# Performance work log

Hardware: AMD Instinct MI355X
Metric: run time of the kernel (lower is better)

Reference implementation:

```python
import jax, jax.numpy as jnp
import numpy as np

N_NODES = 50000
N_EDGES = 800000
D = 256            # node_feat_size
D_EDGE = 16        # edge_feat_size (unused in forward math, as in the original)
G_FEAT = 200       # graph_feat_size
N_TASKS = 1
N_GRAPHS = 512


def _p(key, shape):
    return jax.random.normal(key, shape, dtype=jnp.float32) * 0.05


def setup_inputs() -> dict:
    key = jax.random.key(0)
    ks = jax.random.split(key, 24)
    inp = {
        'node_feats_1': jax.random.normal(ks[0], (N_NODES, D), dtype=jnp.float32),
        'edge_feats_1': jax.random.normal(ks[1], (N_EDGES, D_EDGE), dtype=jnp.float32),
        'node_feats_2': jax.random.normal(ks[2], (N_NODES, D), dtype=jnp.float32),
        'edge_feats_2': jax.random.normal(ks[3], (N_EDGES, D_EDGE), dtype=jnp.float32),
        'src_1': jax.random.randint(ks[4], (N_EDGES,), 0, N_NODES, dtype=jnp.int32),
        'dst_1': jax.random.randint(ks[5], (N_EDGES,), 0, N_NODES, dtype=jnp.int32),
        'graph_ids_1': jnp.sort(jax.random.randint(ks[6], (N_NODES,), 0, N_GRAPHS, dtype=jnp.int32)),
        'src_2': jax.random.randint(ks[7], (N_EDGES,), 0, N_NODES, dtype=jnp.int32),
        'dst_2': jax.random.randint(ks[8], (N_EDGES,), 0, N_NODES, dtype=jnp.int32),
        'graph_ids_2': jnp.sort(jax.random.randint(ks[9], (N_NODES,), 0, N_GRAPHS, dtype=jnp.int32)),
        # GCN layer 1 params (GraphConv weight/bias + residual Linear)
        'W1': _p(ks[10], (D, D)), 'b1': jnp.zeros((D,), jnp.float32),
        'Wr1': _p(ks[11], (D, D)), 'br1': jnp.zeros((D,), jnp.float32),
        # GCN layer 2 params
        'W2': _p(ks[12], (D, D)), 'b2': jnp.zeros((D,), jnp.float32),
        'Wr2': _p(ks[13], (D, D)), 'br2': jnp.zeros((D,), jnp.float32),
        # Readout 1 MLP
        'Ri1': _p(ks[14], (D, D)), 'rbi1': jnp.zeros((D,), jnp.float32),
        'Ro1': _p(ks[15], (D, G_FEAT)), 'rbo1': jnp.zeros((G_FEAT,), jnp.float32),
        # Readout 2 MLP
        'Ri2': _p(ks[16], (D, D)), 'rbi2': jnp.zeros((D,), jnp.float32),
        'Ro2': _p(ks[17], (D, G_FEAT)), 'rbo2': jnp.zeros((G_FEAT,), jnp.float32),
        # Predictor
        'Wp': _p(ks[18], (G_FEAT, N_TASKS)), 'bp': jnp.zeros((N_TASKS,), jnp.float32),
    }
    return inp


def _gcn_layer(h, src, dst, W, b, Wr, br):
    # DGL GraphConv, norm='none': project, aggregate (sum src->dst), bias, relu
    hW = h @ W                                             # [N, D]
    agg = jax.ops.segment_sum(jnp.take(hW, src, axis=0), dst, num_segments=N_NODES)
    conv = jax.nn.relu(agg + b)
    # residual branch: activation(Linear(h))
    res = jax.nn.relu(h @ Wr + br)
    return conv + res                                      # dropout=0, no batchnorm


def _readout(h, graph_ids, Wi, bi, Wo, bo):
    # MLPNodeReadout: Linear -> relu -> Linear, then sum over nodes per graph
    h = jax.nn.relu(h @ Wi + bi)
    h = h @ Wo + bo                                        # [N, G_FEAT]
    return jax.ops.segment_sum(h, graph_ids, num_segments=N_GRAPHS)


def reference(node_feats_1, edge_feats_1, node_feats_2, edge_feats_2,
              src_1, dst_1, graph_ids_1, src_2, dst_2, graph_ids_2,
              W1, b1, Wr1, br1, W2, b2, Wr2, br2,
              Ri1, rbi1, Ro1, rbo1, Ri2, rbi2, Ro2, rbo2, Wp, bp):
    h1 = _gcn_layer(node_feats_1, src_1, dst_1, W1, b1, Wr1, br1)
    g1 = _readout(h1, graph_ids_1, Ri1, rbi1, Ro1, rbo1)
    h2 = _gcn_layer(node_feats_2, src_2, dst_2, W2, b2, Wr2, br2)
    g2 = _readout(h2, graph_ids_2, Ri2, rbi2, Ro2, rbo2)
    g = g1 + g2                                            # [G, G_FEAT]
    return (g @ Wp + bp).reshape(-1)                       # [G * n_tasks]
```

## Files before the change

### kernel.cpp

```cpp
#include <hip/hip_runtime.h>

#define NN 50000
#define NE 800000
#define DD 256
#define GFEAT 200
#define NG 512

typedef __bf16 bf16;
typedef bf16 bf16x4 __attribute__((ext_vector_type(4)));
typedef bf16 bf16x8 __attribute__((ext_vector_type(8)));
typedef float f32x4 __attribute__((ext_vector_type(4)));

__device__ __forceinline__ void gl_lds16(const bf16* g, bf16* l) {
    __builtin_amdgcn_global_load_lds(
        (const __attribute__((address_space(1))) uint32_t*)(g),
        (__attribute__((address_space(3))) uint32_t*)(l), 16, 0, 0);
}

__device__ __forceinline__ bf16x8 frag_ld64(const bf16* s, int R, int C) {
    return *(const bf16x8*)&s[R * 64 + ((C ^ ((R >> 1) & 7)) << 3)];
}

#define EPI_STRIDE 136

__global__ __launch_bounds__(256) void conv_w8_kernel(
    const float* __restrict__ w0, const float* __restrict__ w1,
    const float* __restrict__ w2, const float* __restrict__ w3,
    const float* __restrict__ w4, const float* __restrict__ w5,
    const float* __restrict__ w6, const float* __restrict__ w7,
    bf16* __restrict__ out_base) {
    const float* ws[8] = {w0, w1, w2, w3, w4, w5, w6, w7};
    const int Ns[8] = {DD, DD, DD, GFEAT, DD, DD, DD, GFEAT};
    int m = blockIdx.y;
    const float* in = ws[m];
    int N = Ns[m];
    int idx = blockIdx.x * 256 + threadIdx.x;
    int n = idx >> 8, k = idx & 255;
    float v = (n < N) ? in[k * N + n] : 0.f;
    out_base[(size_t)m * 65536 + idx] = (bf16)v;
}

__global__ __launch_bounds__(256) void zero_g_kernel(float* __restrict__ G0,
                                                     float* __restrict__ G1) {
    float* G = blockIdx.y ? G1 : G0;
    int i = blockIdx.x * 256 + threadIdx.x;
    if (i < NG * GFEAT) G[i] = 0.f;
}

#define NBKT   128
#define NPB    391
#define NCHUNK 256
#define CE     ((NE + NCHUNK - 1) / NCHUNK)

__global__ __launch_bounds__(256) void csr_coarse_hist_kernel(
    const int* __restrict__ d0, const int* __restrict__ d1,
    int* __restrict__ cnt0, int* __restrict__ cnt1) {
    const int blk = blockIdx.x, t = threadIdx.x;
    const int* dst = blockIdx.y ? d1 : d0;
    int* cnt = blockIdx.y ? cnt1 : cnt0;
    __shared__ int hist[NBKT];
    if (t < NBKT) hist[t] = 0;
    __syncthreads();
    const int e0 = blk * CE;
    const int e1 = (e0 + CE < NE) ? e0 + CE : NE;
    for (int e = e0 + t; e < e1; e += 256)
        atomicAdd(&hist[dst[e] / NPB], 1);
    __syncthreads();
    if (t < NBKT) cnt[t * NCHUNK + blk] = hist[t];
}

__global__ __launch_bounds__(1024) void csr_scan_kernel(
    int* __restrict__ cnt0, int* __restrict__ cnt1,
    int* __restrict__ offs0, int* __restrict__ offs1) {
    int* cnt = blockIdx.y ? cnt1 : cnt0;
    const int t = threadIdx.x;
    const int PER = (NBKT * NCHUNK) / 1024;
    int v[PER];
    int sum = 0;
    const int base = t * PER;
#pragma unroll
    for (int i = 0; i < PER; i += 4) {
        int4 q = *(const int4*)&cnt[base + i];
        v[i] = q.x; v[i + 1] = q.y; v[i + 2] = q.z; v[i + 3] = q.w;
        sum += q.x + q.y + q.z + q.w;
    }
    __shared__ int s[1024];
    s[t] = sum;
    __syncthreads();
    for (int off = 1; off < 1024; off <<= 1) {
        int a = (t >= off) ? s[t - off] : 0;
        __syncthreads();
        s[t] += a;
        __syncthreads();
    }
    int run = s[t] - sum;
#pragma unroll
    for (int i = 0; i < PER; i++) { int c = v[i]; cnt[base + i] = run; run += c; }
    if (t == 0) (blockIdx.y ? offs1 : offs0)[NN] = NE;
}

__global__ __launch_bounds__(256) void csr_partition_kernel(
    const int* __restrict__ sA, const int* __restrict__ sB,
    const int* __restrict__ d0, const int* __restrict__ d1,
    const int* __restrict__ cnt0, const int* __restrict__ cnt1,
    int2* __restrict__ eb0, int2* __restrict__ eb1) {
    const int blk = blockIdx.x, t = threadIdx.x;
    const int* src = blockIdx.y ? sB : sA;
    const int* dst = blockIdx.y ? d1 : d0;
    const int* cnt = blockIdx.y ? cnt1 : cnt0;
    int2* eb = blockIdx.y ? eb1 : eb0;
    __shared__ int cur[NBKT];
    if (t < NBKT) cur[t] = cnt[t * NCHUNK + blk];
    __syncthreads();
    const int e0 = blk * CE;
    const int e1 = (e0 + CE < NE) ? e0 + CE : NE;
    for (int e = e0 + t; e < e1; e += 256) {
        int d = dst[e], s = src[e];
        int pos = atomicAdd(&cur[d / NPB], 1);
        eb[pos] = make_int2(s, d);
    }
}

__global__ __launch_bounds__(512) void csr_bucket_sort_kernel(
    const int* __restrict__ cnt0, const int* __restrict__ cnt1,
    const int2* __restrict__ eb0, const int2* __restrict__ eb1,
    int* __restrict__ offs0, int* __restrict__ offs1,
    int* __restrict__ csr0, int* __restrict__ csr1) {
    const int b = blockIdx.x, t = threadIdx.x;
    const int* cnt = blockIdx.y ? cnt1 : cnt0;
    const int2* eb = blockIdx.y ? eb1 : eb0;
    int* offs = blockIdx.y ? offs1 : offs0;
    int* csr = blockIdx.y ? csr1 : csr0;
    const int lo = b * NPB;
    const int ncnt = (NN - lo < NPB) ? (NN - lo) : NPB;
    const int beg = cnt[b * NCHUNK];
    const int end = (b == NBKT - 1) ? NE : cnt[(b + 1) * NCHUNK];

    __shared__ int hist[NPB];
    __shared__ int s[512];
    if (t < NPB) hist[t] = 0;
    __syncthreads();
    for (int i = beg + t; i < end; i += 512)
        atomicAdd(&hist[eb[i].y - lo], 1);
    __syncthreads();

    int h = (t < NPB) ? hist[t] : 0;
    s[t] = h;
    __syncthreads();
    for (int off = 1; off < 512; off <<= 1) {
        int a = (t >= off) ? s[t - off] : 0;
        __syncthreads();
        s[t] += a;
        __syncthreads();
    }
    int excl = s[t] - h;
    __syncthreads();
    if (t < NPB) hist[t] = excl;
    if (t < ncnt) offs[lo + t] = beg + excl;
    __syncthreads();

    for (int i = beg + t; i < end; i += 512) {
        int2 v = eb[i];
        int pos = atomicAdd(&hist[v.y - lo], 1);
        csr[beg + pos] = v.x;
    }
}


__global__ __launch_bounds__(512) void mfma_gemm2_kernel(
    const bf16* __restrict__ A0, const bf16* __restrict__ A1,
    const bf16* __restrict__ Bt0, const bf16* __restrict__ Bt1,
    const float* __restrict__ bias0, const float* __restrict__ bias1,
    bf16* __restrict__ out0, bf16* __restrict__ out1,
    int M, int Nb, int do_relu) {
    const int lid = blockIdx.x;
    const int r8 = lid & 7, cc = (lid >> 3) & 1, g = lid >> 4;
    const int row_blk = g * 8 + r8;
    if (row_blk * 256 >= M) return;
    const bf16* A = blockIdx.y ? A1 : A0;
    const bf16* Bt = blockIdx.y ? Bt1 : Bt0;
    const float* bias = blockIdx.y ? bias1 : bias0;
    bf16* out = blockIdx.y ? out1 : out0;

    __shared__ bf16 smem[24576];
    bf16* As = smem;
    bf16* Bs = smem + 16384;

    const int t    = threadIdx.x;
    const int lane = t & 63;
    const int w    = t >> 6;
    const int row0 = row_blk * 256;
    const int col0 = cc * 128;

    f32x4 acc[4][4] = {};
    const int wm = (w >> 1) * 64, wn = (w & 1) * 64;
    const int fm = lane & 15, fC = lane >> 4;

    for (int k0 = 0; k0 < 256; k0 += 64) {
#pragma unroll
        for (int r = 0; r < 4; r++) {
            int flat = r * 512 + t;
            int fr = flat >> 3, fc = flat & 7;
            int fcg = fc ^ ((fr >> 1) & 7);
            int arow = row0 + fr;
            if (arow > M - 1) arow = M - 1;
            gl_lds16(&A[(size_t)arow * 256 + k0 + fcg * 8], &As[flat * 8]);
        }
#pragma unroll
        for (int r = 0; r < 2; r++) {
            int flat = r * 512 + t;
            int fr = flat >> 3, fc = flat & 7;
            int fcg = fc ^ ((fr >> 1) & 7);
            int brow = col0 + fr;
            gl_lds16(&Bt[(size_t)brow * 256 + k0 + fcg * 8], &Bs[flat * 8]);
        }
        __syncthreads();
#pragma unroll
        for (int s = 0; s < 2; s++) {
            bf16x8 af[4], bfr[4];
#pragma unroll
            for (int i = 0; i < 4; i++) af[i] = frag_ld64(As, wm + i * 16 + fm, s * 4 + fC);
#pragma unroll
            for (int i = 0; i < 4; i++) bfr[i] = frag_ld64(Bs, wn + i * 16 + fm, s * 4 + fC);
#pragma unroll
            for (int i = 0; i < 4; i++)
#pragma unroll
                for (int j = 0; j < 4; j++)
                    acc[i][j] = __builtin_amdgcn_mfma_f32_16x16x32_bf16(af[i], bfr[j], acc[i][j], 0, 0, 0);
        }
        __syncthreads();
    }

    float bv[4];
#pragma unroll
    for (int j = 0; j < 4; j++) {
        int col = col0 + wn + fm + j * 16;
        bv[j] = (col < Nb) ? bias[col] : 0.f;
    }

#pragma unroll
    for (int p = 0; p < 4; p++) {
        if ((w >> 1) == p) {
#pragma unroll
            for (int i = 0; i < 4; i++)
#pragma unroll
                for (int j = 0; j < 4; j++)
#pragma unroll
                    for (int r2 = 0; r2 < 4; r2++) {
                        int rl = i * 16 + (lane >> 4) * 4 + r2;
                        int cl = wn + fm + j * 16;
                        float v = acc[i][j][r2] + bv[j];
                        if (do_relu) v = fmaxf(v, 0.f);
                        smem[rl * EPI_STRIDE + cl] = (bf16)v;
                    }
        }
        __syncthreads();
#pragma unroll
        for (int q = 0; q < 2; q++) {
            int flat = q * 512 + t;
            int rl = flat >> 4, seg = flat & 15;
            int grow = row0 + p * 64 + rl;
            if (grow < M)
                *(bf16x8*)&out[(size_t)grow * 256 + col0 + seg * 8] =
                    *(const bf16x8*)&smem[rl * EPI_STRIDE + seg * 8];
        }
        __syncthreads();
    }
}

__global__ __launch_bounds__(512) void mfma_gemm_fusedconv2_kernel(
    const float* __restrict__ X0, const float* __restrict__ X1,
    const bf16* __restrict__ Bt2_0, const bf16* __restrict__ Bt2_1,
    const float* __restrict__ bh0, const float* __restrict__ bh1,
    bf16* __restrict__ lo0, bf16* __restrict__ lo1,
    bf16* __restrict__ hi0, bf16* __restrict__ hi1, int M) {
    const int lid = blockIdx.x;
    const int r8 = lid & 7, cc = (lid >> 3) & 3, g = lid >> 5;
    const int row_blk = g * 8 + r8;
    if (row_blk * 256 >= M) return;
    const float* Xf = blockIdx.y ? X1 : X0;
    const bf16* Bt2 = blockIdx.y ? Bt2_1 : Bt2_0;
    const float* bias_hi = blockIdx.y ? bh1 : bh0;
    bf16* out_lo = blockIdx.y ? lo1 : lo0;
    bf16* out_hi = blockIdx.y ? hi1 : hi0;

    __shared__ bf16 smem[24576];
    bf16* As = smem;
    bf16* Bs = smem + 16384;

    const int t    = threadIdx.x;
    const int lane = t & 63;
    const int w    = t >> 6;
    const int row0 = row_blk * 256;
    const int col0 = cc * 128;

    f32x4 acc[4][4] = {};
    const int wm = (w >> 1) * 64, wn = (w & 1) * 64;
    const int fm = lane & 15, fC = lane >> 4;

    for (int k0 = 0; k0 < 256; k0 += 64) {
#pragma unroll
        for (int r = 0; r < 2; r++) {
            int flat = r * 512 + t;
            int fr = flat >> 3, fc = flat & 7;
            int fcg = fc ^ ((fr >> 1) & 7);
            int brow = col0 + fr;
            gl_lds16(&Bt2[(size_t)brow * 256 + k0 + fcg * 8], &Bs[flat * 8]);
        }
#pragma unroll
        for (int r = 0; r < 4; r++) {
            int flat = r * 512 + t;
            int fr = flat >> 3, fc = flat & 7;
            int arow = row0 + fr;
            if (arow > M - 1) arow = M - 1;
            const float* gsrc = &Xf[(size_t)arow * 256 + k0 + fc * 8];
            float4 u0 = *(const float4*)gsrc;
            float4 u1 = *(const float4*)(gsrc + 4);
            bf16x8 o;
            o[0] = (bf16)u0.x; o[1] = (bf16)u0.y; o[2] = (bf16)u0.z; o[3] = (bf16)u0.w;
            o[4] = (bf16)u1.x; o[5] = (bf16)u1.y; o[6] = (bf16)u1.z; o[7] = (bf16)u1.w;
            *(bf16x8*)&As[fr * 64 + (fc ^ ((fr >> 1) & 7)) * 8] = o;
        }
        __syncthreads();
#pragma unroll
        for (int s = 0; s < 2; s++) {
            bf16x8 af[4], bfr[4];
#pragma unroll
            for (int i = 0; i < 4; i++) af[i] = frag_ld64(As, wm + i * 16 + fm, s * 4 + fC);
#pragma unroll
            for (int i = 0; i < 4; i++) bfr[i] = frag_ld64(Bs, wn + i * 16 + fm, s * 4 + fC);
#pragma unroll
            for (int i = 0; i < 4; i++)
#pragma unroll
                for (int j = 0; j < 4; j++)
                    acc[i][j] = __builtin_amdgcn_mfma_f32_16x16x32_bf16(af[i], bfr[j], acc[i][j], 0, 0, 0);
        }
        __syncthreads();
    }

    const bool hi = (col0 >= 256);
    bf16* out = hi ? out_hi : out_lo;
    const int cb = hi ? col0 - 256 : col0;

    float bv[4];
#pragma unroll
    for (int j = 0; j < 4; j++) {
        int col = cb + wn + fm + j * 16;
        bv[j] = hi ? bias_hi[col] : 0.f;
    }

#pragma unroll
    for (int p = 0; p < 4; p++) {
        if ((w >> 1) == p) {
#pragma unroll
            for (int i = 0; i < 4; i++)
#pragma unroll
                for (int j = 0; j < 4; j++)
#pragma unroll
                    for (int r2 = 0; r2 < 4; r2++) {
                        int rl = i * 16 + (lane >> 4) * 4 + r2;
                        int cl = wn + fm + j * 16;
                        float v = acc[i][j][r2] + bv[j];
                        if (hi) v = fmaxf(v, 0.f);
                        smem[rl * EPI_STRIDE + cl] = (bf16)v;
                    }
        }
        __syncthreads();
#pragma unroll
        for (int q = 0; q < 2; q++) {
            int flat = q * 512 + t;
            int rl = flat >> 4, seg = flat & 15;
            int grow = row0 + p * 64 + rl;
            if (grow < M)
                *(bf16x8*)&out[(size_t)grow * 256 + cb + seg * 8] =
                    *(const bf16x8*)&smem[rl * EPI_STRIDE + seg * 8];
        }
        __syncthreads();
    }
}

__global__ __launch_bounds__(512) void mfma_gemm_reduce2_kernel(
    const bf16* __restrict__ A0, const bf16* __restrict__ A1,
    const bf16* __restrict__ Bt0, const bf16* __restrict__ Bt1,
    const float* __restrict__ bias0, const float* __restrict__ bias1,
    const int* __restrict__ gid0, const int* __restrict__ gid1,
    float* __restrict__ G0, float* __restrict__ G1, int M, int Nb) {
    const int lid = blockIdx.x;
    const int r8 = lid & 7, cc = (lid >> 3) & 1, g = lid >> 4;
    const int row_blk = g * 8 + r8;
    if (row_blk * 256 >= M) return;
    const bf16* A = blockIdx.y ? A1 : A0;
    const bf16* Bt = blockIdx.y ? Bt1 : Bt0;
    const float* bias = blockIdx.y ? bias1 : bias0;
    const int* gids = blockIdx.y ? gid1 : gid0;
    float* G = blockIdx.y ? G1 : G0;

    __shared__ bf16 smem[24576];
    bf16* As = smem;
    bf16* Bs = smem + 16384;

    const int t    = threadIdx.x;
    const int lane = t & 63;
    const int w    = t >> 6;
    const int row0 = row_blk * 256;
    const int col0 = cc * 128;

    f32x4 acc[4][4] = {};
    const int wm = (w >> 1) * 64, wn = (w & 1) * 64;
    const int fm = lane & 15, fC = lane >> 4;

    for (int k0 = 0; k0 < 256; k0 += 64) {
#pragma unroll
        for (int r = 0; r < 4; r++) {
            int flat = r * 512 + t;
            int fr = flat >> 3, fc = flat & 7;
            int fcg = fc ^ ((fr >> 1) & 7);
            int arow = row0 + fr;
            if (arow > M - 1) arow = M - 1;
            gl_lds16(&A[(size_t)arow * 256 + k0 + fcg * 8], &As[flat * 8]);
        }
#pragma unroll
        for (int r = 0; r < 2; r++) {
            int flat = r * 512 + t;
            int fr = flat >> 3, fc = flat & 7;
            int fcg = fc ^ ((fr >> 1) & 7);
            int brow = col0 + fr;
            gl_lds16(&Bt[(size_t)brow * 256 + k0 + fcg * 8], &Bs[flat * 8]);
        }
        __syncthreads();
#pragma unroll
        for (int s = 0; s < 2; s++) {
            bf16x8 af[4], bfr[4];
#pragma unroll
            for (int i = 0; i < 4; i++) af[i] = frag_ld64(As, wm + i * 16 + fm, s * 4 + fC);
#pragma unroll
            for (int i = 0; i < 4; i++) bfr[i] = frag_ld64(Bs, wn + i * 16 + fm, s * 4 + fC);
#pragma unroll
            for (int i = 0; i < 4; i++)
#pragma unroll
                for (int j = 0; j < 4; j++)
                    acc[i][j] = __builtin_amdgcn_mfma_f32_16x16x32_bf16(af[i], bfr[j], acc[i][j], 0, 0, 0);
        }
        __syncthreads();
    }

    float bv[4];
#pragma unroll
    for (int j = 0; j < 4; j++) {
        int col = col0 + wn + fm + j * 16;
        bv[j] = (col < Nb) ? bias[col] : 0.f;
    }

#pragma unroll
    for (int p = 0; p < 4; p++) {
        if ((w >> 1) == p) {
#pragma unroll
            for (int i = 0; i < 4; i++)
#pragma unroll
                for (int j = 0; j < 4; j++)
#pragma unroll
                    for (int r2 = 0; r2 < 4; r2++) {
                        int rl = i * 16 + (lane >> 4) * 4 + r2;
                        int cl = wn + fm + j * 16;
                        smem[rl * EPI_STRIDE + cl] = (bf16)(acc[i][j][r2] + bv[j]);
                    }
        }
        __syncthreads();
        {
            int c = t & 127, rh = t >> 7;
            int colg = col0 + c;
            if (colg < Nb) {
                float run = 0.f;
                int gprev = -1;
                for (int r = 0; r < 16; r++) {
                    int grow = row0 + p * 64 + rh * 16 + r;
                    if (grow >= M) break;
                    int gg = gids[grow];
                    if (gg != gprev) {
                        if (gprev >= 0) atomicAdd(&G[(size_t)gprev * GFEAT + colg], run);
                        run = 0.f;
                        gprev = gg;
                    }
                    run += (float)smem[(rh * 16 + r) * EPI_STRIDE + c];
                }
                if (gprev >= 0) atomicAdd(&G[(size_t)gprev * GFEAT + colg], run);
            }
        }
        __syncthreads();
    }
}

__global__ __launch_bounds__(256) void agg_combine2_kernel(
    const bf16* __restrict__ hW0, const bf16* __restrict__ hW1,
    const int* __restrict__ csr0, const int* __restrict__ csr1,
    const int* __restrict__ offs0, const int* __restrict__ offs1,
    const float* __restrict__ bias0, const float* __restrict__ bias1,
    const bf16* __restrict__ res0, const bf16* __restrict__ res1,
    bf16* __restrict__ H0, bf16* __restrict__ H1, int n_nodes) {
    const bf16* hW = blockIdx.y ? hW1 : hW0;
    const int* csr_src = blockIdx.y ? csr1 : csr0;
    const int* offsets = blockIdx.y ? offs1 : offs0;
    const float* bias = blockIdx.y ? bias1 : bias0;
    const bf16* res = blockIdx.y ? res1 : res0;
    bf16* H = blockIdx.y ? H1 : H0;

    int wave = threadIdx.x >> 6;
    int lane = threadIdx.x & 63;
    int node = blockIdx.x * 4 + wave;
    if (node >= n_nodes) return;
    int beg = offsets[node], end = offsets[node + 1];
    const int half = lane >> 5;
    const int fo   = (lane & 31) * 8;

    float acc[8] = {};
    int j = beg;
    for (; j + 6 + half < end; j += 8) {
        int s0 = csr_src[j + half];
        int s1 = csr_src[j + 2 + half];
        int s2 = csr_src[j + 4 + half];
        int s3 = csr_src[j + 6 + half];
        bf16x8 v0 = *(const bf16x8*)&hW[(size_t)s0 * DD + fo];
        bf16x8 v1 = *(const bf16x8*)&hW[(size_t)s1 * DD + fo];
        bf16x8 v2 = *(const bf16x8*)&hW[(size_t)s2 * DD + fo];
        bf16x8 v3 = *(const bf16x8*)&hW[(size_t)s3 * DD + fo];
#pragma unroll
        for (int q = 0; q < 8; q++) acc[q] += (float)v0[q];
#pragma unroll
        for (int q = 0; q < 8; q++) acc[q] += (float)v1[q];
#pragma unroll
        for (int q = 0; q < 8; q++) acc[q] += (float)v2[q];
#pragma unroll
        for (int q = 0; q < 8; q++) acc[q] += (float)v3[q];
    }
    for (; j + half < end; j += 2) {
        int s = csr_src[j + half];
        bf16x8 v = *(const bf16x8*)&hW[(size_t)s * DD + fo];
#pragma unroll
        for (int q = 0; q < 8; q++) acc[q] += (float)v[q];
    }
#pragma unroll
    for (int q = 0; q < 8; q++) acc[q] += __shfl_xor(acc[q], 32, 64);

    if (half == 0) {
        float4 b0 = *(const float4*)&bias[fo];
        float4 b1 = *(const float4*)&bias[fo + 4];
        bf16x8 rv = *(const bf16x8*)&res[(size_t)node * DD + fo];
        bf16x8 o;
        o[0] = (bf16)(fmaxf(acc[0] + b0.x, 0.f) + (float)rv[0]);
        o[1] = (bf16)(fmaxf(acc[1] + b0.y, 0.f) + (float)rv[1]);
        o[2] = (bf16)(fmaxf(acc[2] + b0.z, 0.f) + (float)rv[2]);
        o[3] = (bf16)(fmaxf(acc[3] + b0.w, 0.f) + (float)rv[3]);
        o[4] = (bf16)(fmaxf(acc[4] + b1.x, 0.f) + (float)rv[4]);
        o[5] = (bf16)(fmaxf(acc[5] + b1.y, 0.f) + (float)rv[5]);
        o[6] = (bf16)(fmaxf(acc[6] + b1.z, 0.f) + (float)rv[6]);
        o[7] = (bf16)(fmaxf(acc[7] + b1.w, 0.f) + (float)rv[7]);
        *(bf16x8*)&H[(size_t)node * DD + fo] = o;
    }
}

__global__ __launch_bounds__(256) void predictor_kernel(const float* __restrict__ G1,
                                                        const float* __restrict__ G2,
                                                        const float* __restrict__ Wp,
                                                        const float* __restrict__ bp,
                                                        float* __restrict__ out) {
    int i = blockIdx.x * 256 + threadIdx.x;
    if (i >= NG) return;
    float acc = bp[0];
    for (int f = 0; f < GFEAT; f++)
        acc += (G1[i * GFEAT + f] + G2[i * GFEAT + f]) * Wp[f];
    out[i] = acc;
}

extern "C" void kernel_launch(void* const* d_in, const int* in_sizes, int n_in,
                              void* d_out, int out_size, void* d_ws, size_t ws_size,
                              hipStream_t stream) {
    const float* X1   = (const float*)d_in[0];
    const float* X2   = (const float*)d_in[2];
    const int*   src1 = (const int*)d_in[4];
    const int*   dst1 = (const int*)d_in[5];
    const int*   gid1 = (const int*)d_in[6];
    const int*   src2 = (const int*)d_in[7];
    const int*   dst2 = (const int*)d_in[8];
    const int*   gid2 = (const int*)d_in[9];
    const float* W1  = (const float*)d_in[10]; const float* b1  = (const float*)d_in[11];
    const float* Wr1 = (const float*)d_in[12]; const float* br1 = (const float*)d_in[13];
    const float* W2  = (const float*)d_in[14]; const float* b2  = (const float*)d_in[15];
    const float* Wr2 = (const float*)d_in[16]; const float* br2 = (const float*)d_in[17];
    const float* Ri1 = (const float*)d_in[18]; const float* rbi1 = (const float*)d_in[19];
    const float* Ro1 = (const float*)d_in[20]; const float* rbo1 = (const float*)d_in[21];
    const float* Ri2 = (const float*)d_in[22]; const float* rbi2 = (const float*)d_in[23];
    const float* Ro2 = (const float*)d_in[24]; const float* rbo2 = (const float*)d_in[25];
    const float* Wp  = (const float*)d_in[26]; const float* bp  = (const float*)d_in[27];

    const size_t NB = (size_t)NN * DD * sizeof(bf16);
    char* p = (char*)d_ws;
    bf16* H1   = (bf16*)p; p += NB;
    bf16* H2   = (bf16*)p; p += NB;
    bf16* hWR1 = (bf16*)p; p += NB;
    bf16* hWR2 = (bf16*)p; p += NB;
    bf16* res1 = (bf16*)p; p += NB;
    bf16* res2 = (bf16*)p; p += NB;
    float* G1  = (float*)p; p += (size_t)NG * GFEAT * sizeof(float);
    float* G2  = (float*)p; p += (size_t)NG * GFEAT * sizeof(float);
    bf16* Wbase = (bf16*)p; p += 8 * 65536 * sizeof(bf16);
    int* offs1 = (int*)p; p += (NN + 1) * sizeof(int);
    int* offs2 = (int*)p; p += (NN + 1) * sizeof(int);
    int* cnt1  = (int*)p; p += NBKT * NCHUNK * sizeof(int);
    int* cnt2  = (int*)p; p += NBKT * NCHUNK * sizeof(int);
    int* csr1  = (int*)p; p += NE * sizeof(int);
    int* csr2  = (int*)p; p += NE * sizeof(int);
    int2* eb1 = (int2*)hWR1;
    int2* eb2 = (int2*)hWR2;

    zero_g_kernel<<<dim3((NG * GFEAT + 255) / 256, 2), 256, 0, stream>>>(G1, G2);
    conv_w8_kernel<<<dim3(256, 8), 256, 0, stream>>>(W1, Wr1, Ri1, Ro1, W2, Wr2, Ri2, Ro2, Wbase);

    csr_coarse_hist_kernel<<<dim3(NCHUNK, 2), 256, 0, stream>>>(dst1, dst2, cnt1, cnt2);
    csr_scan_kernel<<<dim3(1, 2), 1024, 0, stream>>>(cnt1, cnt2, offs1, offs2);
    csr_partition_kernel<<<dim3(NCHUNK, 2), 256, 0, stream>>>(
        src1, src2, dst1, dst2, cnt1, cnt2, eb1, eb2);
    csr_bucket_sort_kernel<<<dim3(NBKT, 2), 512, 0, stream>>>(
        cnt1, cnt2, eb1, eb2, offs1, offs2, csr1, csr2);

    mfma_gemm_fusedconv2_kernel<<<dim3(25 * 32, 2), 512, 0, stream>>>(
        X1, X2, Wbase + 0 * 65536, Wbase + 4 * 65536, br1, br2,
        hWR1, hWR2, res1, res2, NN);
    agg_combine2_kernel<<<dim3((NN + 3) / 4, 2), 256, 0, stream>>>(
        hWR1, hWR2, csr1, csr2, offs1, offs2, b1, b2, res1, res2, H1, H2, NN);
    mfma_gemm2_kernel<<<dim3(25 * 16, 2), 512, 0, stream>>>(
        H1, H2, Wbase + 2 * 65536, Wbase + 6 * 65536, rbi1, rbi2,
        hWR1, hWR2, NN, DD, 1);
    mfma_gemm_reduce2_kernel<<<dim3(25 * 16, 2), 512, 0, stream>>>(
        hWR1, hWR2, Wbase + 3 * 65536, Wbase + 7 * 65536, rbo1, rbo2,
        gid1, gid2, G1, G2, NN, GFEAT);

    predictor_kernel<<<(NG + 255) / 256, 256, 0, stream>>>(G1, G2, Wp, bp, (float*)d_out);
}
```

Before: 544.6 us.

## Merge CSR build stages with fused GEMM blocks into heterogeneous launches

Zeroing, weight conversion and the coarse histogram are combined into one prep kernel. The CSR partition and bucket-sort stages now share launches with slices of the first fused-conv GEMM, so the graph preprocessing overlaps with tensor-core work. The edge buffer is moved to the H1/H2 scratch so the GEMM outputs in hWR can be written at the same time. Weight conversion now uses an LDS-tiled transpose for coalesced access. The risk is load imbalance inside the mixed grids and extra LDS per block that can lower occupancy for the lightweight blocks.

```diff
diff --git a/kernel.cpp b/kernel.cpp
--- a/kernel.cpp
+++ b/kernel.cpp
@@ -23,50 +23,250 @@
 
 #define EPI_STRIDE 136
 
-__global__ __launch_bounds__(256) void conv_w8_kernel(
-    const float* __restrict__ w0, const float* __restrict__ w1,
-    const float* __restrict__ w2, const float* __restrict__ w3,
-    const float* __restrict__ w4, const float* __restrict__ w5,
-    const float* __restrict__ w6, const float* __restrict__ w7,
-    bf16* __restrict__ out_base) {
-    const float* ws[8] = {w0, w1, w2, w3, w4, w5, w6, w7};
-    const int Ns[8] = {DD, DD, DD, GFEAT, DD, DD, DD, GFEAT};
-    int m = blockIdx.y;
-    const float* in = ws[m];
-    int N = Ns[m];
-    int idx = blockIdx.x * 256 + threadIdx.x;
-    int n = idx >> 8, k = idx & 255;
-    float v = (n < N) ? in[k * N + n] : 0.f;
-    out_base[(size_t)m * 65536 + idx] = (bf16)v;
-}
-
-__global__ __launch_bounds__(256) void zero_g_kernel(float* __restrict__ G0,
-                                                     float* __restrict__ G1) {
-    float* G = blockIdx.y ? G1 : G0;
-    int i = blockIdx.x * 256 + threadIdx.x;
-    if (i < NG * GFEAT) G[i] = 0.f;
-}
-
 #define NBKT   128
 #define NPB    391
 #define NCHUNK 256
 #define CE     ((NE + NCHUNK - 1) / NCHUNK)
 
-__global__ __launch_bounds__(256) void csr_coarse_hist_kernel(
+#define NF1 600
+#define NF2 1000
+
+
+__device__ void d_convw(int bb, const float* const* ws, const int* Ns,
+                        bf16* out_base, char* sm) {
+    const int m = bb >> 4, tile = bb & 15;
+    const int k0 = (tile >> 2) * 64, n0 = (tile & 3) * 64;
+    const float* in = ws[m];
+    const int N = Ns[m];
+    const int t = threadIdx.x;
+    float (*ts)[65] = (float(*)[65])sm;
+#pragma unroll
+    for (int r = 0; r < 8; r++) {
+        int dk = r * 8 + (t >> 6), dn = t & 63;
+        int n = n0 + dn;
+        ts[dk][dn] = (n < N) ? in[(k0 + dk) * N + n] : 0.f;
+    }
+    __syncthreads();
+#pragma unroll
+    for (int r = 0; r < 8; r++) {
+        int dn = r * 8 + (t >> 6), dk = t & 63;
+        out_base[(size_t)m * 65536 + (size_t)(n0 + dn) * 256 + k0 + dk] = (bf16)ts[dk][dn];
+    }
+}
+
+__device__ void d_hist(int hb, const int* d0, const int* d1,
+                       int* cnt0, int* cnt1, char* sm) {
+    const int branch = hb >> 8, blk = hb & 255;
+    const int* dst = branch ? d1 : d0;
+    int* cnt = branch ? cnt1 : cnt0;
+    int* hist = (int*)sm;
+    const int t = threadIdx.x;
+    if (t < NBKT) hist[t] = 0;
+    __syncthreads();
+    const int e0 = blk * CE;
+    const int e1 = (e0 + CE < NE) ? e0 + CE : NE;
+    for (int e = e0 + t; e < e1; e += 512)
+        atomicAdd(&hist[dst[e] / NPB], 1);
+    __syncthreads();
+    if (t < NBKT) cnt[t * NCHUNK + blk] = hist[t];
+}
+
+__device__ void d_partition(int pb, const int* sA, const int* sB,
+                            const int* d0, const int* d1,
+                            const int* cnt0, const int* cnt1,
+                            int2* eb0, int2* eb1, char* sm) {
+    const int branch = pb >> 8, blk = pb & 255;
+    const int* src = branch ? sB : sA;
+    const int* dst = branch ? d1 : d0;
+    const int* cnt = branch ? cnt1 : cnt0;
+    int2* eb = branch ? eb1 : eb0;
+    int* cur = (int*)sm;
+    const int t = threadIdx.x;
+    if (t < NBKT) cur[t] = cnt[t * NCHUNK + blk];
+    __syncthreads();
+    const int e0 = blk * CE;
+    const int e1 = (e0 + CE < NE) ? e0 + CE : NE;
+    for (int e = e0 + t; e < e1; e += 512) {
+        int d = dst[e], s = src[e];
+        int pos = atomicAdd(&cur[d / NPB], 1);
+        eb[pos] = make_int2(s, d);
+    }
+}
+
+__device__ void d_sort(int sb, const int* cnt0, const int* cnt1,
+                       const int2* eb0, const int2* eb1,
+                       int* offs0, int* offs1, int* csr0, int* csr1, char* sm) {
+    const int branch = sb >> 7, b = sb & 127;
+    const int* cnt = branch ? cnt1 : cnt0;
+    const int2* eb = branch ? eb1 : eb0;
+    int* offs = branch ? offs1 : offs0;
+    int* csr = branch ? csr1 : csr0;
+    const int lo = b * NPB;
+    const int ncnt = (NN - lo < NPB) ? (NN - lo) : NPB;
+    const int beg = cnt[b * NCHUNK];
+    const int end = (b == NBKT - 1) ? NE : cnt[(b + 1) * NCHUNK];
+    const int t = threadIdx.x;
+
+    int* hist = (int*)sm;
+    int* s = ((int*)sm) + 400;
+    if (t < NPB) hist[t] = 0;
+    __syncthreads();
+    for (int i = beg + t; i < end; i += 512)
+        atomicAdd(&hist[eb[i].y - lo], 1);
+    __syncthreads();
+
+    int h = (t < NPB) ? hist[t] : 0;
+    s[t] = h;
+    __syncthreads();
+    for (int off = 1; off < 512; off <<= 1) {
+        int a = (t >= off) ? s[t - off] : 0;
+        __syncthreads();
+        s[t] += a;
+        __syncthreads();
+    }
+    int excl = s[t] - h;
+    __syncthreads();
+    if (t < NPB) hist[t] = excl;
+    if (t < ncnt) offs[lo + t] = beg + excl;
+    __syncthreads();
+
+    for (int i = beg + t; i < end; i += 512) {
+        int2 v = eb[i];
+        int pos = atomicAdd(&hist[v.y - lo], 1);
+        csr[beg + pos] = v.x;
+    }
+}
+
+__device__ void d_fusedconv(int f, const float* X0, const float* X1,
+                            const bf16* Bt2_0, const bf16* Bt2_1,
+                            const float* bh0, const float* bh1,
+                            bf16* lo0, bf16* lo1, bf16* hi0, bf16* hi1,
+                            int M, char* smc) {
+    const int br = f & 1, lid = f >> 1;
+    const int r8 = lid & 7, cc = (lid >> 3) & 3, g = lid >> 5;
+    const int row_blk = g * 8 + r8;
+    if (row_blk * 256 >= M) return;
+    const float* Xf = br ? X1 : X0;
+    const bf16* Bt2 = br ? Bt2_1 : Bt2_0;
+    const float* bias_hi = br ? bh1 : bh0;
+    bf16* out_lo = br ? lo1 : lo0;
+    bf16* out_hi = br ? hi1 : hi0;
+
+    bf16* smem = (bf16*)smc;
+    bf16* As = smem;
+    bf16* Bs = smem + 16384;
+
+    const int t    = threadIdx.x;
+    const int lane = t & 63;
+    const int w    = t >> 6;
+    const int row0 = row_blk * 256;
+    const int col0 = cc * 128;
+
+    f32x4 acc[4][4] = {};
+    const int wm = (w >> 1) * 64, wn = (w & 1) * 64;
+    const int fm = lane & 15, fC = lane >> 4;
+
+    for (int k0 = 0; k0 < 256; k0 += 64) {
+#pragma unroll
+        for (int r = 0; r < 2; r++) {
+            int flat = r * 512 + t;
+            int fr = flat >> 3, fc = flat & 7;
+            int fcg = fc ^ ((fr >> 1) & 7);
+            int brow = col0 + fr;
+            gl_lds16(&Bt2[(size_t)brow * 256 + k0 + fcg * 8], &Bs[flat * 8]);
+        }
+#pragma unroll
+        for (int r = 0; r < 4; r++) {
+            int flat = r * 512 + t;
+            int fr = flat >> 3, fc = flat & 7;
+            int arow = row0 + fr;
+            if (arow > M - 1) arow = M - 1;
+            const float* gsrc = &Xf[(size_t)arow * 256 + k0 + fc * 8];
+            float4 u0 = *(const float4*)gsrc;
+            float4 u1 = *(const float4*)(gsrc + 4);
+            bf16x8 o;
+            o[0] = (bf16)u0.x; o[1] = (bf16)u0.y; o[2] = (bf16)u0.z; o[3] = (bf16)u0.w;
+            o[4] = (bf16)u1.x; o[5] = (bf16)u1.y; o[6] = (bf16)u1.z; o[7] = (bf16)u1.w;
+            *(bf16x8*)&As[fr * 64 + ((fc ^ ((fr >> 1) & 7)) << 3)] = o;
+        }
+        __syncthreads();
+#pragma unroll
+        for (int s = 0; s < 2; s++) {
+            bf16x8 af[4], bfr[4];
+#pragma unroll
+            for (int i = 0; i < 4; i++) af[i] = frag_ld64(As, wm + i * 16 + fm, s * 4 + fC);
+#pragma unroll
+            for (int i = 0; i < 4; i++) bfr[i] = frag_ld64(Bs, wn + i * 16 + fm, s * 4 + fC);
+#pragma unroll
+            for (int i = 0; i < 4; i++)
+#pragma unroll
+                for (int j = 0; j < 4; j++)
+                    acc[i][j] = __builtin_amdgcn_mfma_f32_16x16x32_bf16(af[i], bfr[j], acc[i][j], 0, 0, 0);
+        }
+        __syncthreads();
+    }
+
+    const bool hi = (col0 >= 256);
+    bf16* out = hi ? out_hi : out_lo;
+    const int cb = hi ? col0 - 256 : col0;
+
+    float bv[4];
+#pragma unroll
+    for (int j = 0; j < 4; j++) {
+        int col = cb + wn + fm + j * 16;
+        bv[j] = hi ? bias_hi[col] : 0.f;
+    }
+
+#pragma unroll
+    for (int p = 0; p < 4; p++) {
+        if ((w >> 1) == p) {
+#pragma unroll
+            for (int i = 0; i < 4; i++)
+#pragma unroll
+                for (int j = 0; j < 4; j++)
+#pragma unroll
+                    for (int r2 = 0; r2 < 4; r2++) {
+                        int rl = i * 16 + (lane >> 4) * 4 + r2;
+                        int cl = wn + fm + j * 16;
+                        float v = acc[i][j][r2] + bv[j];
+                        if (hi) v = fmaxf(v, 0.f);
+                        smem[rl * EPI_STRIDE + cl] = (bf16)v;
+                    }
+        }
+        __syncthreads();
+#pragma unroll
+        for (int q = 0; q < 2; q++) {
+            int flat = q * 512 + t;
+            int rl = flat >> 4, seg = flat & 15;
+            int grow = row0 + p * 64 + rl;
+            if (grow < M)
+                *(bf16x8*)&out[(size_t)grow * 256 + cb + seg * 8] =
+                    *(const bf16x8*)&smem[rl * EPI_STRIDE + seg * 8];
+        }
+        __syncthreads();
+    }
+}
+
+__global__ __launch_bounds__(512) void k_prep(
+    float* __restrict__ G1, float* __restrict__ G2,
+    const float* w0, const float* w1, const float* w2, const float* w3,
+    const float* w4, const float* w5, const float* w6, const float* w7,
+    bf16* __restrict__ Wbase,
     const int* __restrict__ d0, const int* __restrict__ d1,
     int* __restrict__ cnt0, int* __restrict__ cnt1) {
-    const int blk = blockIdx.x, t = threadIdx.x;
-    const int* dst = blockIdx.y ? d1 : d0;
-    int* cnt = blockIdx.y ? cnt1 : cnt0;
-    __shared__ int hist[NBKT];
-    if (t < NBKT) hist[t] = 0;
-    __syncthreads();
-    const int e0 = blk * CE;
-    const int e1 = (e0 + CE < NE) ? e0 + CE : NE;
-    for (int e = e0 + t; e < e1; e += 256)
-        atomicAdd(&hist[dst[e] / NPB], 1);
-    __syncthreads();
-    if (t < NBKT) cnt[t * NCHUNK + blk] = hist[t];
+    __shared__ __align__(16) char sm[16704];
+    const int b = blockIdx.x;
+    if (b < 400) {
+        int i = b * 512 + threadIdx.x;
+        if (i < NG * GFEAT) G1[i] = 0.f;
+        else if (i < 2 * NG * GFEAT) G2[i - NG * GFEAT] = 0.f;
+    } else if (b < 528) {
+        const float* ws[8] = {w0, w1, w2, w3, w4, w5, w6, w7};
+        const int Ns[8] = {DD, DD, DD, GFEAT, DD, DD, DD, GFEAT};
+        d_convw(b - 400, ws, Ns, Wbase, sm);
+    } else {
+        d_hist(b - 528, d0, d1, cnt0, cnt1, sm);
+    }
 }
 
 __global__ __launch_bounds__(1024) void csr_scan_kernel(
@@ -99,73 +299,38 @@
     if (t == 0) (blockIdx.y ? offs1 : offs0)[NN] = NE;
 }
 
-__global__ __launch_bounds__(256) void csr_partition_kernel(
+__global__ __launch_bounds__(512) void k_part_gemm(
     const int* __restrict__ sA, const int* __restrict__ sB,
     const int* __restrict__ d0, const int* __restrict__ d1,
     const int* __restrict__ cnt0, const int* __restrict__ cnt1,
-    int2* __restrict__ eb0, int2* __restrict__ eb1) {
-    const int blk = blockIdx.x, t = threadIdx.x;
-    const int* src = blockIdx.y ? sB : sA;
-    const int* dst = blockIdx.y ? d1 : d0;
-    const int* cnt = blockIdx.y ? cnt1 : cnt0;
-    int2* eb = blockIdx.y ? eb1 : eb0;
-    __shared__ int cur[NBKT];
-    if (t < NBKT) cur[t] = cnt[t * NCHUNK + blk];
-    __syncthreads();
-    const int e0 = blk * CE;
-    const int e1 = (e0 + CE < NE) ? e0 + CE : NE;
-    for (int e = e0 + t; e < e1; e += 256) {
-        int d = dst[e], s = src[e];
-        int pos = atomicAdd(&cur[d / NPB], 1);
-        eb[pos] = make_int2(s, d);
-    }
-}
-
-__global__ __launch_bounds__(512) void csr_bucket_sort_kernel(
+    int2* __restrict__ eb0, int2* __restrict__ eb1,
+    const float* __restrict__ X0, const float* __restrict__ X1,
+    const bf16* __restrict__ Bt2_0, const bf16* __restrict__ Bt2_1,
+    const float* __restrict__ bh0, const float* __restrict__ bh1,
+    bf16* __restrict__ lo0, bf16* __restrict__ lo1,
+    bf16* __restrict__ hi0, bf16* __restrict__ hi1, int M) {
+    __shared__ __align__(16) char sm[49152];
+    const int b = blockIdx.x;
+    if (b < 512) d_partition(b, sA, sB, d0, d1, cnt0, cnt1, eb0, eb1, sm);
+    else d_fusedconv(b - 512, X0, X1, Bt2_0, Bt2_1, bh0, bh1, lo0, lo1, hi0, hi1, M, sm);
+}
+
+__global__ __launch_bounds__(512) void k_sort_gemm(
     const int* __restrict__ cnt0, const int* __restrict__ cnt1,
     const int2* __restrict__ eb0, const int2* __restrict__ eb1,
     int* __restrict__ offs0, int* __restrict__ offs1,
-    int* __restrict__ csr0, int* __restrict__ csr1) {
-    const int b = blockIdx.x, t = threadIdx.x;
-    const int* cnt = blockIdx.y ? cnt1 : cnt0;
-    const int2* eb = blockIdx.y ? eb1 : eb0;
-    int* offs = blockIdx.y ? offs1 : offs0;
-    int* csr = blockIdx.y ? csr1 : csr0;
-    const int lo = b * NPB;
-    const int ncnt = (NN - lo < NPB) ? (NN - lo) : NPB;
-    const int beg = cnt[b * NCHUNK];
-    const int end = (b == NBKT - 1) ? NE : cnt[(b + 1) * NCHUNK];
-
-    __shared__ int hist[NPB];
-    __shared__ int s[512];
-    if (t < NPB) hist[t] = 0;
-    __syncthreads();
-    for (int i = beg + t; i < end; i += 512)
-        atomicAdd(&hist[eb[i].y - lo], 1);
-    __syncthreads();
-
-    int h = (t < NPB) ? hist[t] : 0;
-    s[t] = h;
-    __syncthreads();
-    for (int off = 1; off < 512; off <<= 1) {
-        int a = (t >= off) ? s[t - off] : 0;
-        __syncthreads();
-        s[t] += a;
-        __syncthreads();
-    }
-    int excl = s[t] - h;
-    __syncthreads();
-    if (t < NPB) hist[t] = excl;
-    if (t < ncnt) offs[lo + t] = beg + excl;
-    __syncthreads();
-
-    for (int i = beg + t; i < end; i += 512) {
-        int2 v = eb[i];
-        int pos = atomicAdd(&hist[v.y - lo], 1);
-        csr[beg + pos] = v.x;
-    }
-}
-
+    int* __restrict__ csr0, int* __restrict__ csr1,
+    const float* __restrict__ X0, const float* __restrict__ X1,
+    const bf16* __restrict__ Bt2_0, const bf16* __restrict__ Bt2_1,
+    const float* __restrict__ bh0, const float* __restrict__ bh1,
+    bf16* __restrict__ lo0, bf16* __restrict__ lo1,
+    bf16* __restrict__ hi0, bf16* __restrict__ hi1, int M) {
+    __shared__ __align__(16) char sm[49152];
+    const int b = blockIdx.x;
+    if (b < 256) d_sort(b, cnt0, cnt1, eb0, eb1, offs0, offs1, csr0, csr1, sm);
+    else d_fusedconv(b - 256 + NF1, X0, X1, Bt2_0, Bt2_1, bh0, bh1,
+                     lo0, lo1, hi0, hi1, M, sm);
+}
 
 __global__ __launch_bounds__(512) void mfma_gemm2_kernel(
     const bf16* __restrict__ A0, const bf16* __restrict__ A1,
@@ -262,117 +427,6 @@
             int grow = row0 + p * 64 + rl;
             if (grow < M)
                 *(bf16x8*)&out[(size_t)grow * 256 + col0 + seg * 8] =
-                    *(const bf16x8*)&smem[rl * EPI_STRIDE + seg * 8];
-        }
-        __syncthreads();
-    }
-}
-
-__global__ __launch_bounds__(512) void mfma_gemm_fusedconv2_kernel(
-    const float* __restrict__ X0, const float* __restrict__ X1,
-    const bf16* __restrict__ Bt2_0, const bf16* __restrict__ Bt2_1,
-    const float* __restrict__ bh0, const float* __restrict__ bh1,
-    bf16* __restrict__ lo0, bf16* __restrict__ lo1,
-    bf16* __restrict__ hi0, bf16* __restrict__ hi1, int M) {
-    const int lid = blockIdx.x;
-    const int r8 = lid & 7, cc = (lid >> 3) & 3, g = lid >> 5;
-    const int row_blk = g * 8 + r8;
-    if (row_blk * 256 >= M) return;
-    const float* Xf = blockIdx.y ? X1 : X0;
-    const bf16* Bt2 = blockIdx.y ? Bt2_1 : Bt2_0;
-    const float* bias_hi = blockIdx.y ? bh1 : bh0;
-    bf16* out_lo = blockIdx.y ? lo1 : lo0;
-    bf16* out_hi = blockIdx.y ? hi1 : hi0;
-
-    __shared__ bf16 smem[24576];
-    bf16* As = smem;
-    bf16* Bs = smem + 16384;
-
-    const int t    = threadIdx.x;
-    const int lane = t & 63;
-    const int w    = t >> 6;
-    const int row0 = row_blk * 256;
-    const int col0 = cc * 128;
-
-    f32x4 acc[4][4] = {};
-    const int wm = (w >> 1) * 64, wn = (w & 1) * 64;
-    const int fm = lane & 15, fC = lane >> 4;
-
-    for (int k0 = 0; k0 < 256; k0 += 64) {
-#pragma unroll
-        for (int r = 0; r < 2; r++) {
-            int flat = r * 512 + t;
-            int fr = flat >> 3, fc = flat & 7;
-            int fcg = fc ^ ((fr >> 1) & 7);
-            int brow = col0 + fr;
-            gl_lds16(&Bt2[(size_t)brow * 256 + k0 + fcg * 8], &Bs[flat * 8]);
-        }
-#pragma unroll
-        for (int r = 0; r < 4; r++) {
-            int flat = r * 512 + t;
-            int fr = flat >> 3, fc = flat & 7;
-            int arow = row0 + fr;
-            if (arow > M - 1) arow = M - 1;
-            const float* gsrc = &Xf[(size_t)arow * 256 + k0 + fc * 8];
-            float4 u0 = *(const float4*)gsrc;
-            float4 u1 = *(const float4*)(gsrc + 4);
-            bf16x8 o;
-            o[0] = (bf16)u0.x; o[1] = (bf16)u0.y; o[2] = (bf16)u0.z; o[3] = (bf16)u0.w;
-            o[4] = (bf16)u1.x; o[5] = (bf16)u1.y; o[6] = (bf16)u1.z; o[7] = (bf16)u1.w;
-            *(bf16x8*)&As[fr * 64 + (fc ^ ((fr >> 1) & 7)) * 8] = o;
-        }
-        __syncthreads();
-#pragma unroll
-        for (int s = 0; s < 2; s++) {
-            bf16x8 af[4], bfr[4];
-#pragma unroll
-            for (int i = 0; i < 4; i++) af[i] = frag_ld64(As, wm + i * 16 + fm, s * 4 + fC);
-#pragma unroll
-            for (int i = 0; i < 4; i++) bfr[i] = frag_ld64(Bs, wn + i * 16 + fm, s * 4 + fC);
-#pragma unroll
-            for (int i = 0; i < 4; i++)
-#pragma unroll
-                for (int j = 0; j < 4; j++)
-                    acc[i][j] = __builtin_amdgcn_mfma_f32_16x16x32_bf16(af[i], bfr[j], acc[i][j], 0, 0, 0);
-        }
-        __syncthreads();
-    }
-
-    const bool hi = (col0 >= 256);
-    bf16* out = hi ? out_hi : out_lo;
-    const int cb = hi ? col0 - 256 : col0;
-
-    float bv[4];
-#pragma unroll
-    for (int j = 0; j < 4; j++) {
-        int col = cb + wn + fm + j * 16;
-        bv[j] = hi ? bias_hi[col] : 0.f;
-    }
-
-#pragma unroll
-    for (int p = 0; p < 4; p++) {
-        if ((w >> 1) == p) {
-#pragma unroll
-            for (int i = 0; i < 4; i++)
-#pragma unroll
-                for (int j = 0; j < 4; j++)
-#pragma unroll
-                    for (int r2 = 0; r2 < 4; r2++) {
-                        int rl = i * 16 + (lane >> 4) * 4 + r2;
-                        int cl = wn + fm + j * 16;
-                        float v = acc[i][j][r2] + bv[j];
-                        if (hi) v = fmaxf(v, 0.f);
-                        smem[rl * EPI_STRIDE + cl] = (bf16)v;
-                    }
-        }
-        __syncthreads();
-#pragma unroll
-        for (int q = 0; q < 2; q++) {
-            int flat = q * 512 + t;
-            int rl = flat >> 4, seg = flat & 15;
-            int grow = row0 + p * 64 + rl;
-            if (grow < M)
-                *(bf16x8*)&out[(size_t)grow * 256 + cb + seg * 8] =
                     *(const bf16x8*)&smem[rl * EPI_STRIDE + seg * 8];
         }
         __syncthreads();
@@ -609,20 +663,18 @@
     int* cnt2  = (int*)p; p += NBKT * NCHUNK * sizeof(int);
     int* csr1  = (int*)p; p += NE * sizeof(int);
     int* csr2  = (int*)p; p += NE * sizeof(int);
-    int2* eb1 = (int2*)hWR1;
-    int2* eb2 = (int2*)hWR2;
-
-    zero_g_kernel<<<dim3((NG * GFEAT + 255) / 256, 2), 256, 0, stream>>>(G1, G2);
-    conv_w8_kernel<<<dim3(256, 8), 256, 0, stream>>>(W1, Wr1, Ri1, Ro1, W2, Wr2, Ri2, Ro2, Wbase);
-
-    csr_coarse_hist_kernel<<<dim3(NCHUNK, 2), 256, 0, stream>>>(dst1, dst2, cnt1, cnt2);
+    int2* eb1 = (int2*)H1;
+    int2* eb2 = (int2*)H2;
+
+    k_prep<<<1040, 512, 0, stream>>>(G1, G2, W1, Wr1, Ri1, Ro1, W2, Wr2, Ri2, Ro2,
+                                     Wbase, dst1, dst2, cnt1, cnt2);
     csr_scan_kernel<<<dim3(1, 2), 1024, 0, stream>>>(cnt1, cnt2, offs1, offs2);
-    csr_partition_kernel<<<dim3(NCHUNK, 2), 256, 0, stream>>>(
-        src1, src2, dst1, dst2, cnt1, cnt2, eb1, eb2);
-    csr_bucket_sort_kernel<<<dim3(NBKT, 2), 512, 0, stream>>>(
-        cnt1, cnt2, eb1, eb2, offs1, offs2, csr1, csr2);
-
-    mfma_gemm_fusedconv2_kernel<<<dim3(25 * 32, 2), 512, 0, stream>>>(
+    k_part_gemm<<<512 + NF1, 512, 0, stream>>>(
+        src1, src2, dst1, dst2, cnt1, cnt2, eb1, eb2,
+        X1, X2, Wbase + 0 * 65536, Wbase + 4 * 65536, br1, br2,
+        hWR1, hWR2, res1, res2, NN);
+    k_sort_gemm<<<256 + NF2, 512, 0, stream>>>(
+        cnt1, cnt2, eb1, eb2, offs1, offs2, csr1, csr2,
         X1, X2, Wbase + 0 * 65536, Wbase + 4 * 65536, br1, br2,
         hWR1, hWR2, res1, res2, NN);
     agg_combine2_kernel<<<dim3((NN + 3) / 4, 2), 256, 0, stream>>>(
@@ -633,6 +685,5 @@
     mfma_gemm_reduce2_kernel<<<dim3(25 * 16, 2), 512, 0, stream>>>(
         hWR1, hWR2, Wbase + 3 * 65536, Wbase + 7 * 65536, rbo1, rbo2,
         gid1, gid2, G1, G2, NN, GFEAT);
-
     predictor_kernel<<<(NG + 255) / 256, 256, 0, stream>>>(G1, G2, Wp, bp, (float*)d_out);
 }
```

Result: slower. 622.8 us (+14.4%).

## Map aggregation branches to XCD halves and tile the weight transpose through LDS

Applied to the files above, without the earlier changes.

The aggregation kernel now runs as a flat 1D grid. Block indices are remapped so that blocks landing on XCDs 0-3 handle branch 0 and XCDs 4-7 handle branch 1. The aim is to keep each branch's gathered hW rows inside the L2 caches of fewer XCDs, which should raise cache reuse of the random neighbor reads. Separately, the weight fp32-to-bf16 transpose kernel now uses 64x64 LDS tiles so that both its reads and its writes are coalesced. This relies on the round-robin XCD block dispatch assumption and could leave the load uneven across XCDs.

```diff
diff --git a/kernel.cpp b/kernel.cpp
--- a/kernel.cpp
+++ b/kernel.cpp
@@ -23,7 +23,7 @@
 
 #define EPI_STRIDE 136
 
-__global__ __launch_bounds__(256) void conv_w8_kernel(
+__global__ __launch_bounds__(256) void conv_w8t_kernel(
     const float* __restrict__ w0, const float* __restrict__ w1,
     const float* __restrict__ w2, const float* __restrict__ w3,
     const float* __restrict__ w4, const float* __restrict__ w5,
@@ -31,13 +31,25 @@
     bf16* __restrict__ out_base) {
     const float* ws[8] = {w0, w1, w2, w3, w4, w5, w6, w7};
     const int Ns[8] = {DD, DD, DD, GFEAT, DD, DD, DD, GFEAT};
-    int m = blockIdx.y;
+    const int m = blockIdx.x >> 4;
+    const int tile = blockIdx.x & 15;
+    const int k0 = (tile >> 2) * 64, n0 = (tile & 3) * 64;
     const float* in = ws[m];
-    int N = Ns[m];
-    int idx = blockIdx.x * 256 + threadIdx.x;
-    int n = idx >> 8, k = idx & 255;
-    float v = (n < N) ? in[k * N + n] : 0.f;
-    out_base[(size_t)m * 65536 + idx] = (bf16)v;
+    const int N = Ns[m];
+    const int t = threadIdx.x;
+    __shared__ float ts[64][65];
+#pragma unroll
+    for (int r = 0; r < 16; r++) {
+        int dk = r * 4 + (t >> 6), dn = t & 63;
+        int n = n0 + dn;
+        ts[dk][dn] = (n < N) ? in[(k0 + dk) * N + n] : 0.f;
+    }
+    __syncthreads();
+#pragma unroll
+    for (int r = 0; r < 16; r++) {
+        int dn = r * 4 + (t >> 6), dk = t & 63;
+        out_base[(size_t)m * 65536 + (size_t)(n0 + dn) * 256 + k0 + dk] = (bf16)ts[dk][dn];
+    }
 }
 
 __global__ __launch_bounds__(256) void zero_g_kernel(float* __restrict__ G0,
@@ -165,7 +177,6 @@
         csr[beg + pos] = v.x;
     }
 }
-
 
 __global__ __launch_bounds__(512) void mfma_gemm2_kernel(
     const bf16* __restrict__ A0, const bf16* __restrict__ A1,
@@ -319,7 +330,7 @@
             bf16x8 o;
             o[0] = (bf16)u0.x; o[1] = (bf16)u0.y; o[2] = (bf16)u0.z; o[3] = (bf16)u0.w;
             o[4] = (bf16)u1.x; o[5] = (bf16)u1.y; o[6] = (bf16)u1.z; o[7] = (bf16)u1.w;
-            *(bf16x8*)&As[fr * 64 + (fc ^ ((fr >> 1) & 7)) * 8] = o;
+            *(bf16x8*)&As[fr * 64 + ((fc ^ ((fr >> 1) & 7)) << 3)] = o;
         }
         __syncthreads();
 #pragma unroll
@@ -497,16 +508,21 @@
     const float* __restrict__ bias0, const float* __restrict__ bias1,
     const bf16* __restrict__ res0, const bf16* __restrict__ res1,
     bf16* __restrict__ H0, bf16* __restrict__ H1, int n_nodes) {
-    const bf16* hW = blockIdx.y ? hW1 : hW0;
-    const int* csr_src = blockIdx.y ? csr1 : csr0;
-    const int* offsets = blockIdx.y ? offs1 : offs0;
-    const float* bias = blockIdx.y ? bias1 : bias0;
-    const bf16* res = blockIdx.y ? res1 : res0;
-    bf16* H = blockIdx.y ? H1 : H0;
+    const int x = blockIdx.x;
+    const int xcd = x & 7;
+    const int branch = xcd >> 2;
+    const int local_blk = (x >> 3) * 4 + (xcd & 3);
+
+    const bf16* hW = branch ? hW1 : hW0;
+    const int* csr_src = branch ? csr1 : csr0;
+    const int* offsets = branch ? offs1 : offs0;
+    const float* bias = branch ? bias1 : bias0;
+    const bf16* res = branch ? res1 : res0;
+    bf16* H = branch ? H1 : H0;
 
     int wave = threadIdx.x >> 6;
     int lane = threadIdx.x & 63;
-    int node = blockIdx.x * 4 + wave;
+    int node = local_blk * 4 + wave;
     if (node >= n_nodes) return;
     int beg = offsets[node], end = offsets[node + 1];
     const int half = lane >> 5;
@@ -613,7 +629,7 @@
     int2* eb2 = (int2*)hWR2;
 
     zero_g_kernel<<<dim3((NG * GFEAT + 255) / 256, 2), 256, 0, stream>>>(G1, G2);
-    conv_w8_kernel<<<dim3(256, 8), 256, 0, stream>>>(W1, Wr1, Ri1, Ro1, W2, Wr2, Ri2, Ro2, Wbase);
+    conv_w8t_kernel<<<128, 256, 0, stream>>>(W1, Wr1, Ri1, Ro1, W2, Wr2, Ri2, Ro2, Wbase);
 
     csr_coarse_hist_kernel<<<dim3(NCHUNK, 2), 256, 0, stream>>>(dst1, dst2, cnt1, cnt2);
     csr_scan_kernel<<<dim3(1, 2), 1024, 0, stream>>>(cnt1, cnt2, offs1, offs2);
@@ -625,7 +641,7 @@
     mfma_gemm_fusedconv2_kernel<<<dim3(25 * 32, 2), 512, 0, stream>>>(
         X1, X2, Wbase + 0 * 65536, Wbase + 4 * 65536, br1, br2,
         hWR1, hWR2, res1, res2, NN);
-    agg_combine2_kernel<<<dim3((NN + 3) / 4, 2), 256, 0, stream>>>(
+    agg_combine2_kernel<<<25000, 256, 0, stream>>>(
         hWR1, hWR2, csr1, csr2, offs1, offs2, b1, b2, res1, res2, H1, H2, NN);
     mfma_gemm2_kernel<<<dim3(25 * 16, 2), 512, 0, stream>>>(
         H1, H2, Wbase + 2 * 65536, Wbase + 6 * 65536, rbi1, rbi2,
```

Result: no change. 538.9 us (-1.0%).
